# Optimization experiments

Measured on AMD Instinct MI355X. Metric: run time of the kernel, lower is better.

The kernel has to match this reference:

```python
import jax, jax.numpy as jnp
import numpy as np

# DeformConv hyperparameters (from init_kwargs)
KH, KW = 3, 3
STRIDE, PAD, DIL = 1, 1, 1
GROUPS, DG = 1, 1  # groups=1, deformable_groups=1
B, C, H, W = 4, 64, 128, 128
O = 64
HO = (H + 2 * PAD - (DIL * (KH - 1) + 1)) // STRIDE + 1  # 128
WO = (W + 2 * PAD - (DIL * (KW - 1) + 1)) // STRIDE + 1  # 128


def setup_inputs() -> dict:
    key = jax.random.key(0)
    k1, k2, k3, k4 = jax.random.split(key, 4)
    x = jax.random.normal(k1, (B, C, H, W), dtype=jnp.float32)
    # offset channels: dg * K * 2, ordered (y, x) per kernel tap (DCNv1 CUDA layout)
    offset = jax.random.normal(k2, (B, 2 * DG * KH * KW, HO, WO), dtype=jnp.float32)
    fan_in = C * KH * KW
    weight = jax.random.normal(k3, (O, C // GROUPS, KH, KW), dtype=jnp.float32) / np.sqrt(fan_in)
    bias = jax.random.normal(k4, (O,), dtype=jnp.float32) * 0.01
    return {"x": x, "offset": offset, "weight": weight, "bias": bias}


def _deform_sample(x, offset):
    """Bilinear-sample x at deformed kernel tap locations.
    Returns [B, C, K, HO, WO] where K = KH*KW."""
    K = KH * KW
    Cg = C // DG
    # offset -> [B, DG, K, 2, HO, WO]; channel layout: dg*2*K, pairs (y, x)
    off = offset.reshape(B, DG, K, 2, HO, WO)
    off_y, off_x = off[:, :, :, 0], off[:, :, :, 1]  # [B, DG, K, HO, WO]

    ki = (jnp.arange(K) // KW).astype(jnp.float32)  # kernel row
    kj = (jnp.arange(K) % KW).astype(jnp.float32)   # kernel col
    base_h = (jnp.arange(HO) * STRIDE - PAD).astype(jnp.float32)
    base_w = (jnp.arange(WO) * STRIDE - PAD).astype(jnp.float32)

    # sampling positions [B, DG, K, HO, WO]
    py = off_y + (ki * DIL)[None, None, :, None, None] + base_h[None, None, None, :, None]
    px = off_x + (kj * DIL)[None, None, :, None, None] + base_w[None, None, None, None, :]

    y0f = jnp.floor(py)
    x0f = jnp.floor(px)
    ly = py - y0f
    lx = px - x0f
    hy = 1.0 - ly
    hx = 1.0 - lx
    y0 = y0f.astype(jnp.int32)
    x0 = x0f.astype(jnp.int32)
    y1 = y0 + 1
    x1 = x0 + 1

    flat = x.reshape(B, DG, Cg, H * W)

    def gather(yi, xi, wgt):
        valid = (yi >= 0) & (yi < H) & (xi >= 0) & (xi < W)
        idx = jnp.clip(yi, 0, H - 1) * W + jnp.clip(xi, 0, W - 1)
        idx = idx.reshape(B, DG, 1, K * HO * WO)
        v = jnp.take_along_axis(flat, idx, axis=-1).reshape(B, DG, Cg, K, HO, WO)
        return v * (wgt * valid.astype(wgt.dtype))[:, :, None]

    val = (gather(y0, x0, hy * hx) + gather(y0, x1, hy * lx)
           + gather(y1, x0, ly * hx) + gather(y1, x1, ly * lx))
    return val.reshape(B, C, K, HO, WO)


def reference(x, offset, weight, bias):
    sampled = _deform_sample(x, offset)              # [B, C, K, HO, WO]
    w = weight.reshape(O, C, KH * KW)                # groups = 1
    out = jnp.einsum('bckhw,ock->bohw', sampled, w)  # im2col + GEMM
    return out + bias[None, :, None, None]
```

## Files before the change

### kernel.cpp

```cpp
#include <hip/hip_runtime.h>
#include <hip/hip_fp16.h>


#define B_  4
#define C_  64
#define H_  128
#define W_  128
#define O_  64
#define HO_ 128
#define WO_ 128
#define NCH 8
#define NCHUNK 8
#define NG  20
#define KSTEPS 5
#define NT_ 32
#define NTASK (9 * NT_)
#define SG  10
#define SBUF (SG * NT_ * 8)

typedef __attribute__((ext_vector_type(8))) short short8;
typedef __attribute__((ext_vector_type(4))) float f32x4;

__device__ __forceinline__ unsigned short f2bf(float f) {
    unsigned int u = __builtin_bit_cast(unsigned int, f);
    return (unsigned short)((u + 0x7FFFu + ((u >> 16) & 1u)) >> 16);
}
__device__ __forceinline__ float bf2f(unsigned short h) {
    unsigned int u = ((unsigned int)h) << 16;
    return __builtin_bit_cast(float, u);
}

__global__ __launch_bounds__(256)
void prep(const float* __restrict__ x, const float* __restrict__ w,
          __half* __restrict__ xt, unsigned short* __restrict__ wt3) {
    const int tid = threadIdx.x;
    if (blockIdx.x < 2048) {
        int t = blockIdx.x * 256 + tid;
        int xc = t & 127;
        int y  = (t >> 7) & 127;
        int ch = (t >> 14) & 7;
        int b  = t >> 17;
        const float* xp = x + (((size_t)(b * C_ + ch * NCH) * H_) + y) * W_ + xc;
        union { __half h[8]; float4 v; } pk;
#pragma unroll
        for (int e = 0; e < 8; ++e) pk.h[e] = __float2half_rn(xp[e * H_ * W_]);
        *(float4*)(xt + (size_t)t * 8) = pk.v;
    } else {
        int t = (blockIdx.x - 2048) * 256 + tid;
        if (t >= NCHUNK * NG * O_) return;
        int o  = t & 63;
        int g  = (t >> 6) % NG;
        int ch = (t >> 6) / NG;
        union { unsigned short u[8]; short8 v; } pk;
        if (g >= 18) {
#pragma unroll
            for (int e = 0; e < 8; ++e) pk.u[e] = 0;
        } else {
            int k = (g < 9) ? g : g - 9;
#pragma unroll
            for (int e = 0; e < 8; ++e) {
                float wf = w[(o * C_ + ch * NCH + e) * 9 + k];
                unsigned short wh = f2bf(wf);
                pk.u[e] = (g < 9) ? wh : f2bf(wf - bf2f(wh));
            }
        }
        *(short8*)(wt3 + (size_t)t * 8) = pk.v;
    }
}

__global__ __launch_bounds__(256, 4)
void dcn_mfma(const __half* __restrict__ xt, const float* __restrict__ off,
              const unsigned short* __restrict__ wt3, const float* __restrict__ bias,
              float* __restrict__ out) {
    __shared__ __align__(16) unsigned short sS[2 * SBUF];

    const int tid = threadIdx.x;
    const int bid = blockIdx.x;
    const int w4  = bid & 3;
    const int ho  = (bid >> 2) & (HO_ - 1);
    const int b   = bid >> 9;
    const int woB = w4 * NT_;

    int   a0_[2], a1_[2];
    float ua_[2], ub_[2], va_[2], vb_[2];
#pragma unroll
    for (int r = 0; r < 2; ++r) {
        int task = tid + r * 256;
        int tk = (task < NTASK) ? task : 0;
        int k  = tk >> 5;
        int wo = (tk & (NT_ - 1)) + woB;
        int ki = k / 3, kj = k - 3 * ki;
        float oy = off[(((b * 18) + 2 * k    ) * HO_ + ho) * WO_ + wo];
        float ox = off[(((b * 18) + 2 * k + 1) * HO_ + ho) * WO_ + wo];
        float py = (float)(ho - 1 + ki) + oy;
        float px = (float)(wo - 1 + kj) + ox;
        float y0f = floorf(py), x0f = floorf(px);
        int   y0 = (int)y0f,   x0 = (int)x0f;
        float ly = py - y0f,   lx = px - x0f;
        float hy = 1.f - ly,   hx = 1.f - lx;
        int y1 = y0 + 1, x1 = x0 + 1;
        float vy0 = (y0 >= 0 && y0 < H_) ? 1.f : 0.f;
        float vy1 = (y1 >= 0 && y1 < H_) ? 1.f : 0.f;
        float vx0 = (x0 >= 0 && x0 < W_) ? 1.f : 0.f;
        float vx1 = (x1 >= 0 && x1 < W_) ? 1.f : 0.f;
        int cy0 = min(max(y0, 0), H_ - 1), cy1 = min(max(y1, 0), H_ - 1);
        int cx0 = min(max(x0, 0), W_ - 1), cx1 = min(max(x1, 0), W_ - 1);
        int ax  = min(max(x0, 0), W_ - 2);
        float w00 = hy * hx * vy0 * vx0;
        float w01 = hy * lx * vy0 * vx1;
        float w10 = ly * hx * vy1 * vx0;
        float w11 = ly * lx * vy1 * vx1;
        float s0 = (cx0 != ax) ? 1.f : 0.f;
        float s1 = (cx1 != ax) ? 1.f : 0.f;
        a0_[r] = cy0 * W_ + ax;
        a1_[r] = cy1 * W_ + ax;
        ua_[r] = w00 * (1.f - s0) + w01 * (1.f - s1);
        ub_[r] = w00 * s0 + w01 * s1;
        va_[r] = w10 * (1.f - s0) + w11 * (1.f - s1);
        vb_[r] = w10 * s0 + w11 * s1;
    }

    if (tid < 128) {
        ((unsigned int*)&sS[9 * NT_ * 8])[tid]        = 0u;
        ((unsigned int*)&sS[SBUF + 9 * NT_ * 8])[tid] = 0u;
    }

    auto sample = [&](int ch, unsigned short* buf) {
        const float4* xc = (const float4*)(xt + ((size_t)(b * NCHUNK + ch)) * (H_ * W_ * 8));
#pragma unroll
        for (int r = 0; r < 2; ++r) {
            int task = tid + r * 256;
            if (task < NTASK) {
                int k  = task >> 5;
                int wo = task & (NT_ - 1);
                const int a0 = a0_[r], a1 = a1_[r];
                const float ua = ua_[r], ub = ub_[r], va = va_[r], vb = vb_[r];
                union H8 { float4 v; __half2 h2[4]; } q00, q01, q10, q11;
                q00.v = xc[a0];
                q01.v = xc[a0 + 1];
                q10.v = xc[a1];
                q11.v = xc[a1 + 1];
                union { unsigned short u[8]; short8 v; } ph;
#pragma unroll
                for (int j = 0; j < 4; ++j) {
                    float2 A0 = __half22float2(q00.h2[j]);
                    float2 B0 = __half22float2(q01.h2[j]);
                    float2 A1 = __half22float2(q10.h2[j]);
                    float2 B1 = __half22float2(q11.h2[j]);
                    float sx = ua * A0.x + ub * B0.x + va * A1.x + vb * B1.x;
                    float sy = ua * A0.y + ub * B0.y + va * A1.y + vb * B1.y;
                    ph.u[2 * j]     = f2bf(sx);
                    ph.u[2 * j + 1] = f2bf(sy);
                }
                *(short8*)&buf[(k * NT_ + wo) * 8] = ph.v;
            }
        }
    };

    const int lane = tid & 63;
    const int wv   = tid >> 6;
    const int quad = lane >> 4;
    const int l15  = lane & 15;

    f32x4 acc[2];
    acc[0] = (f32x4){0.f, 0.f, 0.f, 0.f};
    acc[1] = (f32x4){0.f, 0.f, 0.f, 0.f};

    sample(0, sS);

    for (int ch = 0; ch < NCHUNK; ++ch) {
        __syncthreads();
        if (ch + 1 < NCHUNK) sample(ch + 1, sS + ((ch + 1) & 1) * SBUF);
        const unsigned short* buf = sS + (ch & 1) * SBUF;
        const unsigned short* wc  = wt3 + (size_t)(ch * NG) * O_ * 8;
#pragma unroll
        for (int ks = 0; ks < KSTEPS; ++ks) {
            int g  = ks * 4 + quad;
            int gb = (g < 9) ? g : ((g < 18) ? g - 9 : 9);
            short8 afr = *(const short8*)(wc + (size_t)(g * O_ + wv * 16 + l15) * 8);
#pragma unroll
            for (int nt = 0; nt < 2; ++nt) {
                short8 bfr = *(const short8*)&buf[(gb * NT_ + nt * 16 + l15) * 8];
                acc[nt] = __builtin_amdgcn_mfma_f32_16x16x32_bf16(afr, bfr, acc[nt], 0, 0, 0);
            }
        }
    }

#pragma unroll
    for (int nt = 0; nt < 2; ++nt) {
        int wo = woB + nt * 16 + l15;
#pragma unroll
        for (int rg = 0; rg < 4; ++rg) {
            int o = wv * 16 + quad * 4 + rg;
            out[(((size_t)(b * O_ + o)) * HO_ + ho) * WO_ + wo] = acc[nt][rg] + bias[o];
        }
    }
}

extern "C" void kernel_launch(void* const* d_in, const int* in_sizes, int n_in,
                              void* d_out, int out_size, void* d_ws, size_t ws_size,
                              hipStream_t stream) {
    const float* x    = (const float*)d_in[0];
    const float* off  = (const float*)d_in[1];
    const float* w    = (const float*)d_in[2];
    const float* bias = (const float*)d_in[3];
    float* out = (float*)d_out;

    unsigned short* wt3 = (unsigned short*)d_ws;
    __half* xt = (__half*)((char*)d_ws + 262144);

    hipLaunchKernelGGL(prep, dim3(2048 + 40), dim3(256), 0, stream, x, w, xt, wt3);
    hipLaunchKernelGGL(dcn_mfma, dim3(B_ * HO_ * (WO_ / NT_)), dim3(256), 0, stream,
                       xt, off, wt3, bias, out);
}
```

Before: 116.5 us.

## Switch to fp16 MFMA without split weights, fp16 blending, and register-prefetched gathers

Replaces the bf16 hi/lo split-weight GEMM (20 groups, 5 k-steps) with a single fp16 weight copy (12 groups, 3 k-steps), which cuts MFMA count and weight traffic. The bilinear blend now runs in packed half2 FMAs, and its outputs are written to shared memory as fp16 with no bf16 conversion. Gathers for the next chunk are issued into registers before the current chunk's MFMAs so their latency overlaps compute. Wave-to-tile mapping changes so each wave shares one B fragment across two output tiles. The trade-off is lower precision from fp16 weights and fp16 accumulation inside the blend, plus higher register pressure from the prefetched gather values.

```diff
diff --git a/kernel.cpp b/kernel.cpp
--- a/kernel.cpp
+++ b/kernel.cpp
@@ -9,30 +9,22 @@
 #define O_  64
 #define HO_ 128
 #define WO_ 128
-#define NCH 8
 #define NCHUNK 8
-#define NG  20
-#define KSTEPS 5
+#define NGW 12
+#define KSTEPS 3
 #define NT_ 32
 #define NTASK (9 * NT_)
 #define SG  10
 #define SBUF (SG * NT_ * 8)
 
-typedef __attribute__((ext_vector_type(8))) short short8;
+typedef _Float16 half8 __attribute__((ext_vector_type(8)));
 typedef __attribute__((ext_vector_type(4))) float f32x4;
 
-__device__ __forceinline__ unsigned short f2bf(float f) {
-    unsigned int u = __builtin_bit_cast(unsigned int, f);
-    return (unsigned short)((u + 0x7FFFu + ((u >> 16) & 1u)) >> 16);
-}
-__device__ __forceinline__ float bf2f(unsigned short h) {
-    unsigned int u = ((unsigned int)h) << 16;
-    return __builtin_bit_cast(float, u);
-}
+union H8 { float4 v; __half2 h2[4]; half8 v8; };
 
 __global__ __launch_bounds__(256)
 void prep(const float* __restrict__ x, const float* __restrict__ w,
-          __half* __restrict__ xt, unsigned short* __restrict__ wt3) {
+          __half* __restrict__ xt, __half* __restrict__ wt) {
     const int tid = threadIdx.x;
     if (blockIdx.x < 2048) {
         int t = blockIdx.x * 256 + tid;
@@ -40,39 +32,31 @@
         int y  = (t >> 7) & 127;
         int ch = (t >> 14) & 7;
         int b  = t >> 17;
-        const float* xp = x + (((size_t)(b * C_ + ch * NCH) * H_) + y) * W_ + xc;
+        const float* xp = x + (((size_t)(b * C_ + ch * 8) * H_) + y) * W_ + xc;
         union { __half h[8]; float4 v; } pk;
 #pragma unroll
         for (int e = 0; e < 8; ++e) pk.h[e] = __float2half_rn(xp[e * H_ * W_]);
         *(float4*)(xt + (size_t)t * 8) = pk.v;
     } else {
         int t = (blockIdx.x - 2048) * 256 + tid;
-        if (t >= NCHUNK * NG * O_) return;
+        if (t >= NCHUNK * NGW * O_) return;
         int o  = t & 63;
-        int g  = (t >> 6) % NG;
-        int ch = (t >> 6) / NG;
-        union { unsigned short u[8]; short8 v; } pk;
-        if (g >= 18) {
-#pragma unroll
-            for (int e = 0; e < 8; ++e) pk.u[e] = 0;
-        } else {
-            int k = (g < 9) ? g : g - 9;
-#pragma unroll
-            for (int e = 0; e < 8; ++e) {
-                float wf = w[(o * C_ + ch * NCH + e) * 9 + k];
-                unsigned short wh = f2bf(wf);
-                pk.u[e] = (g < 9) ? wh : f2bf(wf - bf2f(wh));
-            }
-        }
-        *(short8*)(wt3 + (size_t)t * 8) = pk.v;
+        int g  = (t >> 6) % NGW;
+        int ch = (t >> 6) / NGW;
+        union { __half h[8]; float4 v; } pk;
+#pragma unroll
+        for (int e = 0; e < 8; ++e)
+            pk.h[e] = (g < 9) ? __float2half_rn(w[(o * C_ + ch * 8 + e) * 9 + g])
+                              : __half(0.0f);
+        *(float4*)(wt + (size_t)t * 8) = pk.v;
     }
 }
 
 __global__ __launch_bounds__(256, 4)
 void dcn_mfma(const __half* __restrict__ xt, const float* __restrict__ off,
-              const unsigned short* __restrict__ wt3, const float* __restrict__ bias,
+              const __half* __restrict__ wt, const float* __restrict__ bias,
               float* __restrict__ out) {
-    __shared__ __align__(16) unsigned short sS[2 * SBUF];
+    __shared__ __align__(16) _Float16 sS[2 * SBUF];
 
     const int tid = threadIdx.x;
     const int bid = blockIdx.x;
@@ -81,8 +65,8 @@
     const int b   = bid >> 9;
     const int woB = w4 * NT_;
 
-    int   a0_[2], a1_[2];
-    float ua_[2], ub_[2], va_[2], vb_[2];
+    int a0_[2], a1_[2];
+    __half2 ua2_[2], ub2_[2], va2_[2], vb2_[2];
 #pragma unroll
     for (int r = 0; r < 2; ++r) {
         int task = tid + r * 256;
@@ -114,10 +98,10 @@
         float s1 = (cx1 != ax) ? 1.f : 0.f;
         a0_[r] = cy0 * W_ + ax;
         a1_[r] = cy1 * W_ + ax;
-        ua_[r] = w00 * (1.f - s0) + w01 * (1.f - s1);
-        ub_[r] = w00 * s0 + w01 * s1;
-        va_[r] = w10 * (1.f - s0) + w11 * (1.f - s1);
-        vb_[r] = w10 * s0 + w11 * s1;
+        ua2_[r] = __float2half2_rn(w00 * (1.f - s0) + w01 * (1.f - s1));
+        ub2_[r] = __float2half2_rn(w00 * s0 + w01 * s1);
+        va2_[r] = __float2half2_rn(w10 * (1.f - s0) + w11 * (1.f - s1));
+        vb2_[r] = __float2half2_rn(w10 * s0 + w11 * s1);
     }
 
     if (tid < 128) {
@@ -125,40 +109,54 @@
         ((unsigned int*)&sS[SBUF + 9 * NT_ * 8])[tid] = 0u;
     }
 
-    auto sample = [&](int ch, unsigned short* buf) {
+    H8 q00, q01, q10, q11;
+    H8 p00, p01, p10, p11;
+
+    auto issue = [&](int ch) {
         const float4* xc = (const float4*)(xt + ((size_t)(b * NCHUNK + ch)) * (H_ * W_ * 8));
-#pragma unroll
-        for (int r = 0; r < 2; ++r) {
-            int task = tid + r * 256;
-            if (task < NTASK) {
-                int k  = task >> 5;
-                int wo = task & (NT_ - 1);
-                const int a0 = a0_[r], a1 = a1_[r];
-                const float ua = ua_[r], ub = ub_[r], va = va_[r], vb = vb_[r];
-                union H8 { float4 v; __half2 h2[4]; } q00, q01, q10, q11;
-                q00.v = xc[a0];
-                q01.v = xc[a0 + 1];
-                q10.v = xc[a1];
-                q11.v = xc[a1 + 1];
-                union { unsigned short u[8]; short8 v; } ph;
-#pragma unroll
-                for (int j = 0; j < 4; ++j) {
-                    float2 A0 = __half22float2(q00.h2[j]);
-                    float2 B0 = __half22float2(q01.h2[j]);
-                    float2 A1 = __half22float2(q10.h2[j]);
-                    float2 B1 = __half22float2(q11.h2[j]);
-                    float sx = ua * A0.x + ub * B0.x + va * A1.x + vb * B1.x;
-                    float sy = ua * A0.y + ub * B0.y + va * A1.y + vb * B1.y;
-                    ph.u[2 * j]     = f2bf(sx);
-                    ph.u[2 * j + 1] = f2bf(sy);
-                }
-                *(short8*)&buf[(k * NT_ + wo) * 8] = ph.v;
+        q00.v = xc[a0_[0]];      q01.v = xc[a0_[0] + 1];
+        q10.v = xc[a1_[0]];      q11.v = xc[a1_[0] + 1];
+        if (tid < 32) {
+            p00.v = xc[a0_[1]];  p01.v = xc[a0_[1] + 1];
+            p10.v = xc[a1_[1]];  p11.v = xc[a1_[1] + 1];
+        }
+    };
+
+    auto blend = [&](int bufi) {
+        _Float16* buf = sS + bufi * SBUF;
+        {
+            int k = tid >> 5, wo = tid & (NT_ - 1);
+            H8 s;
+#pragma unroll
+            for (int j = 0; j < 4; ++j) {
+                __half2 t0 = __hmul2(ua2_[0], q00.h2[j]);
+                t0 = __hfma2(ub2_[0], q01.h2[j], t0);
+                t0 = __hfma2(va2_[0], q10.h2[j], t0);
+                t0 = __hfma2(vb2_[0], q11.h2[j], t0);
+                s.h2[j] = t0;
             }
+            *(half8*)&buf[(k * NT_ + wo) * 8] = s.v8;
+        }
+        if (tid < 32) {
+            int task = tid + 256;
+            int k = task >> 5, wo = task & (NT_ - 1);
+            H8 s;
+#pragma unroll
+            for (int j = 0; j < 4; ++j) {
+                __half2 t0 = __hmul2(ua2_[1], p00.h2[j]);
+                t0 = __hfma2(ub2_[1], p01.h2[j], t0);
+                t0 = __hfma2(va2_[1], p10.h2[j], t0);
+                t0 = __hfma2(vb2_[1], p11.h2[j], t0);
+                s.h2[j] = t0;
+            }
+            *(half8*)&buf[(k * NT_ + wo) * 8] = s.v8;
         }
     };
 
     const int lane = tid & 63;
     const int wv   = tid >> 6;
+    const int ow   = wv & 1;
+    const int nw   = wv >> 1;
     const int quad = lane >> 4;
     const int l15  = lane & 15;
 
@@ -166,33 +164,35 @@
     acc[0] = (f32x4){0.f, 0.f, 0.f, 0.f};
     acc[1] = (f32x4){0.f, 0.f, 0.f, 0.f};
 
-    sample(0, sS);
+    issue(0);
 
     for (int ch = 0; ch < NCHUNK; ++ch) {
+        blend(ch & 1);
         __syncthreads();
-        if (ch + 1 < NCHUNK) sample(ch + 1, sS + ((ch + 1) & 1) * SBUF);
-        const unsigned short* buf = sS + (ch & 1) * SBUF;
-        const unsigned short* wc  = wt3 + (size_t)(ch * NG) * O_ * 8;
+        if (ch + 1 < NCHUNK) issue(ch + 1);
+
+        const __half*   wc  = wt + (size_t)(ch * NGW) * O_ * 8;
+        const _Float16* buf = sS + (ch & 1) * SBUF;
 #pragma unroll
         for (int ks = 0; ks < KSTEPS; ++ks) {
             int g  = ks * 4 + quad;
-            int gb = (g < 9) ? g : ((g < 18) ? g - 9 : 9);
-            short8 afr = *(const short8*)(wc + (size_t)(g * O_ + wv * 16 + l15) * 8);
-#pragma unroll
-            for (int nt = 0; nt < 2; ++nt) {
-                short8 bfr = *(const short8*)&buf[(gb * NT_ + nt * 16 + l15) * 8];
-                acc[nt] = __builtin_amdgcn_mfma_f32_16x16x32_bf16(afr, bfr, acc[nt], 0, 0, 0);
+            int gb = (g < 9) ? g : 9;
+            half8 bfr = *(const half8*)&buf[(gb * NT_ + nw * 16 + l15) * 8];
+#pragma unroll
+            for (int ot = 0; ot < 2; ++ot) {
+                half8 afr = *(const half8*)(wc + (size_t)(g * O_ + ow * 32 + ot * 16 + l15) * 8);
+                acc[ot] = __builtin_amdgcn_mfma_f32_16x16x32_f16(afr, bfr, acc[ot], 0, 0, 0);
             }
         }
     }
 
 #pragma unroll
-    for (int nt = 0; nt < 2; ++nt) {
-        int wo = woB + nt * 16 + l15;
+    for (int ot = 0; ot < 2; ++ot) {
+        int wo = woB + nw * 16 + l15;
 #pragma unroll
         for (int rg = 0; rg < 4; ++rg) {
-            int o = wv * 16 + quad * 4 + rg;
-            out[(((size_t)(b * O_ + o)) * HO_ + ho) * WO_ + wo] = acc[nt][rg] + bias[o];
+            int o = ow * 32 + ot * 16 + quad * 4 + rg;
+            out[(((size_t)(b * O_ + o)) * HO_ + ho) * WO_ + wo] = acc[ot][rg] + bias[o];
         }
     }
 }
@@ -206,10 +206,10 @@
     const float* bias = (const float*)d_in[3];
     float* out = (float*)d_out;
 
-    unsigned short* wt3 = (unsigned short*)d_ws;
+    __half* wt = (__half*)d_ws;
     __half* xt = (__half*)((char*)d_ws + 262144);
 
-    hipLaunchKernelGGL(prep, dim3(2048 + 40), dim3(256), 0, stream, x, w, xt, wt3);
+    hipLaunchKernelGGL(prep, dim3(2048 + 24), dim3(256), 0, stream, x, w, xt, wt);
     hipLaunchKernelGGL(dcn_mfma, dim3(B_ * HO_ * (WO_ / NT_)), dim3(256), 0, stream,
-                       xt, off, wt3, bias, out);
+                       xt, off, wt, bias, out);
 }
```

Result: faster. 107.2 us (-8.1%).
